# Kernel tuning notes

Measured on AMD Instinct MI355X. Metric: run time of the kernel, lower is better.

## Reference

```python
import jax, jax.numpy as jnp
import numpy as np

H = 16  # heads
D = 1024  # hidden
HD = D // H
FF = 4096
EPS = 1e-12


def _linear_params(key, d_in, d_out):
    k1, k2 = jax.random.split(key)
    bound = 1.0 / np.sqrt(d_in)
    W = jax.random.uniform(k1, (d_in, d_out), minval=-bound, maxval=bound, dtype=jnp.float32)
    b = jax.random.uniform(k2, (d_out,), minval=-bound, maxval=bound, dtype=jnp.float32)
    return W, b


def setup_inputs() -> dict:
    key = jax.random.key(0)
    ks = jax.random.split(key, 8)
    x = jax.random.normal(ks[0], (4, 2048, D), dtype=jnp.float32)
    mask = jnp.ones((4, 1, 1, 2048), dtype=jnp.int32)
    Wq, bq = _linear_params(ks[1], D, D)
    Wk, bk = _linear_params(ks[2], D, D)
    Wv, bv = _linear_params(ks[3], D, D)
    Wo, bo = _linear_params(ks[4], D, D)
    W1, b1 = _linear_params(ks[5], D, FF)
    W2, b2 = _linear_params(ks[6], FF, D)
    g1 = jnp.ones((D,), jnp.float32); be1 = jnp.zeros((D,), jnp.float32)
    g2 = jnp.ones((D,), jnp.float32); be2 = jnp.zeros((D,), jnp.float32)
    return {"x": x, "mask": mask,
            "Wq": Wq, "bq": bq, "Wk": Wk, "bk": bk, "Wv": Wv, "bv": bv,
            "Wo": Wo, "bo": bo, "W1": W1, "b1": b1, "W2": W2, "b2": b2,
            "g1": g1, "be1": be1, "g2": g2, "be2": be2}


def _layernorm(x, g, b):
    mu = jnp.mean(x, axis=-1, keepdims=True)
    var = jnp.mean(jnp.square(x - mu), axis=-1, keepdims=True)
    return (x - mu) / jnp.sqrt(var + EPS) * g + b


def reference(x, mask, Wq, bq, Wk, bk, Wv, bv, Wo, bo, W1, b1, W2, b2, g1, be1, g2, be2):
    B, L, _ = x.shape
    h = _layernorm(x, g1, be1)
    # [B, H, L, HD]
    q = (h @ Wq + bq).reshape(B, L, H, HD).transpose(0, 2, 1, 3)
    k = (h @ Wk + bk).reshape(B, L, H, HD).transpose(0, 2, 1, 3)
    v = (h @ Wv + bv).reshape(B, L, H, HD).transpose(0, 2, 1, 3)
    scores = jnp.einsum('bhqd,bhkd->bhqk', q, k) / np.sqrt(HD).astype(np.float32)
    scores = jnp.where(mask == 0, jnp.float32(-1e9), scores)
    attn = jax.nn.softmax(scores, axis=-1)  # dropout = identity (eval mode)
    out = jnp.einsum('bhqk,bhkd->bhqd', attn, v)
    out = out.transpose(0, 2, 1, 3).reshape(B, L, D)
    x = x + (out @ Wo + bo)
    h = _layernorm(x, g2, be2)
    ff = jax.nn.gelu(h @ W1 + b1, approximate=False) @ W2 + b2
    return x + ff
```

## Files before the change

kernel.cpp:

```cpp
#include <hip/hip_runtime.h>
#include <stdint.h>

#define D_MODEL 1024
#define NHEAD   16
#define HDIM    64
#define FFDIM   4096
#define BATCH   4
#define SEQ     2048
#define ROWS    (BATCH*SEQ)

typedef unsigned short u16;
typedef __bf16 bf16_t;
typedef bf16_t bf16x8 __attribute__((ext_vector_type(8)));
typedef float  f32x4  __attribute__((ext_vector_type(4)));

#define SCQ 0.18033688011112042f

__device__ __forceinline__ u16 f2bf(float f) {
  union { float f; unsigned u; } v; v.f = f;
  unsigned r = v.u + 0x7fffu + ((v.u >> 16) & 1u);
  return (u16)(r >> 16);
}

__device__ __forceinline__ void gl2lds16(const void* g, void* l) {
  __builtin_amdgcn_global_load_lds((const __attribute__((address_space(1))) void*)g,
                                   (__attribute__((address_space(3))) void*)l, 16, 0, 0);
}

#define MFMA_BF16(a, b, c) __builtin_amdgcn_mfma_f32_16x16x32_bf16((a), (b), (c), 0, 0, 0)
#define EXP2(x) __builtin_amdgcn_exp2f(x)

__global__ __launch_bounds__(256) void ln_kernel(const float* __restrict__ x,
                                                 const float* __restrict__ g,
                                                 const float* __restrict__ be,
                                                 u16* __restrict__ out) {
  __shared__ float red[10];
  int row = blockIdx.x;
  int t = threadIdx.x;
  const float* xr = x + (size_t)row * D_MODEL;
  float4 xv = ((const float4*)xr)[t];
  float s  = xv.x + xv.y + xv.z + xv.w;
  float s2 = xv.x*xv.x + xv.y*xv.y + xv.z*xv.z + xv.w*xv.w;
  for (int d = 32; d > 0; d >>= 1) { s += __shfl_down(s, d); s2 += __shfl_down(s2, d); }
  int wid = t >> 6;
  if ((t & 63) == 0) { red[wid*2] = s; red[wid*2+1] = s2; }
  __syncthreads();
  if (t == 0) {
    float a = 0.f, b2 = 0.f;
    for (int i = 0; i < 4; ++i) { a += red[i*2]; b2 += red[i*2+1]; }
    red[8] = a; red[9] = b2;
  }
  __syncthreads();
  float mu  = red[8] * (1.0f / D_MODEL);
  float var = red[9] * (1.0f / D_MODEL) - mu*mu;
  float rstd = rsqrtf(var + 1e-12f);
  float4 gv = ((const float4*)g)[t];
  float4 bv = ((const float4*)be)[t];
  unsigned long long o =
      (unsigned long long)f2bf((xv.x - mu) * rstd * gv.x + bv.x)
    | ((unsigned long long)f2bf((xv.y - mu) * rstd * gv.y + bv.y) << 16)
    | ((unsigned long long)f2bf((xv.z - mu) * rstd * gv.z + bv.z) << 32)
    | ((unsigned long long)f2bf((xv.w - mu) * rstd * gv.w + bv.w) << 48);
  ((unsigned long long*)out)[(size_t)row * (D_MODEL/4) + t] = o;
}

__global__ __launch_bounds__(256) void wt_kernel(const float* __restrict__ W,
                                                 u16* __restrict__ Wt, int K, int N) {
  __shared__ float tile[32][33];
  int n0 = blockIdx.x * 32, k0 = blockIdx.y * 32;
  int tx = threadIdx.x & 31, ty = threadIdx.x >> 5;
  #pragma unroll
  for (int i = 0; i < 4; ++i) {
    int k = ty + i*8;
    tile[k][tx] = W[(size_t)(k0 + k) * N + n0 + tx];
  }
  __syncthreads();
  #pragma unroll
  for (int i = 0; i < 4; ++i) {
    int n = ty + i*8;
    Wt[(size_t)(n0 + n) * K + k0 + tx] = f2bf(tile[tx][n]);
  }
}

__global__ __launch_bounds__(256) void vtrans_kernel(const u16* __restrict__ vb,
                                                     u16* __restrict__ vt) {
  __shared__ __align__(16) u16 tile[64][80];
  int kb = blockIdx.x * 64;
  int bh = blockIdx.y;
  int b = bh >> 4, h = bh & 15;
  int t = threadIdx.x;
  int key = t >> 2, dq = (t & 3) * 16;
  const u16* src = vb + (size_t)b*SEQ*D_MODEL + (size_t)(kb+key)*D_MODEL + h*HDIM + dq;
  *(bf16x8*)&tile[key][dq]     = *(const bf16x8*)(src);
  *(bf16x8*)&tile[key][dq + 8] = *(const bf16x8*)(src + 8);
  __syncthreads();
  int w = t >> 6, lane = t & 63;
  int kq = w * 16;
  u16 vals[16];
  #pragma unroll
  for (int e = 0; e < 16; ++e) vals[e] = tile[kq + e][lane];
  u16* dst = vt + (size_t)bh * HDIM * SEQ + (size_t)lane * SEQ + kb + kq;
  *(bf16x8*)dst       = *(const bf16x8*)&vals[0];
  *(bf16x8*)(dst + 8) = *(const bf16x8*)&vals[8];
}

__device__ __forceinline__ float gelu_f(float v) {
  return 0.5f * v * (1.0f + erff(v * 0.70710678118654752f));
}

template<int EPI>
__global__ __launch_bounds__(512, 2) void gemm256(const u16* __restrict__ A,
                                                  const u16* __restrict__ Bt,
                                                  const float* __restrict__ bias,
                                                  const float* __restrict__ resid,
                                                  void* __restrict__ outp,
                                                  int M, int N, int K,
                                                  const float* __restrict__ bias2,
                                                  const float* __restrict__ bias3,
                                                  void* __restrict__ out2,
                                                  void* __restrict__ out3) {
  __shared__ __align__(16) u16 sA[3][128*64];
  __shared__ __align__(16) u16 sB[3][256*64];
  const int tid = threadIdx.x;
  const int lane = tid & 63, w = tid >> 6;
  const int r = lane & 15, kg = lane >> 4, r7 = r & 7;
  const int wr = w >> 2, wc = w & 3;

  const int gx = gridDim.x;
  const int nwg = gx * gridDim.y;
  const int orig = blockIdx.y * gx + blockIdx.x;
  const int lid = (orig & 7) * (nwg >> 3) + (orig >> 3);
  const int bm = lid / gx, bn = lid % gx;

  const int NT = K >> 6;

  size_t offA[2], offB[4];
  #pragma unroll
  for (int u = 0; u < 2; ++u) {
    int slot = u*512 + tid;
    int row = slot >> 3, g = slot & 7;
    offA[u] = (size_t)(bm*128 + row) * K + ((g ^ (row & 7)) * 8);
  }
  #pragma unroll
  for (int u = 0; u < 4; ++u) {
    int slot = u*512 + tid;
    int row = slot >> 3, g = slot & 7;
    offB[u] = (size_t)(bn*256 + row) * K + ((g ^ (row & 7)) * 8);
  }

  f32x4 acc[4][4];
  #pragma unroll
  for (int m = 0; m < 4; ++m)
    #pragma unroll
    for (int n = 0; n < 4; ++n) acc[m][n] = f32x4{0.f, 0.f, 0.f, 0.f};

  const float* bsel = bias;
  u16* osel = (u16*)outp;
  int bnl = bn;
  float qscale = 1.0f;
  if (EPI == 3) {
    int sec = bn >> 2;
    bsel = (sec == 0) ? bias : (sec == 1 ? bias2 : bias3);
    osel = (u16*)((sec == 0) ? outp : (sec == 1 ? out2 : out3));
    if (sec == 0) qscale = SCQ;
    bnl = bn & 3;
  }
  float bv4[4];
  #pragma unroll
  for (int n = 0; n < 4; ++n) bv4[n] = bsel[bnl*256 + wc*64 + n*16 + r];

  auto load_frags = [&](bf16x8 (&aa)[4], bf16x8 (&bb)[4], int bbuf, int sl) {
    #pragma unroll
    for (int m = 0; m < 4; ++m)
      aa[m] = *(const bf16x8*)&sA[bbuf][(wr*64 + m*16 + r)*64 + (((sl*4 + kg) ^ r7) * 8)];
    #pragma unroll
    for (int n = 0; n < 4; ++n)
      bb[n] = *(const bf16x8*)&sB[bbuf][(wc*64 + n*16 + r)*64 + (((sl*4 + kg) ^ r7) * 8)];
  };
  auto mfma16 = [&](bf16x8 (&aa)[4], bf16x8 (&bb)[4]) {
    __builtin_amdgcn_s_setprio(1);
    #pragma unroll
    for (int m = 0; m < 4; ++m)
      #pragma unroll
      for (int n = 0; n < 4; ++n)
        acc[m][n] = MFMA_BF16(aa[m], bb[n], acc[m][n]);
    __builtin_amdgcn_s_setprio(0);
  };

  #pragma unroll
  for (int u = 0; u < 2; ++u) gl2lds16(A  + offA[u],      &sA[0][(u*512+tid)*8]);
  #pragma unroll
  for (int u = 0; u < 4; ++u) gl2lds16(Bt + offB[u],      &sB[0][(u*512+tid)*8]);
  #pragma unroll
  for (int u = 0; u < 2; ++u) gl2lds16(A  + offA[u] + 64, &sA[1][(u*512+tid)*8]);
  #pragma unroll
  for (int u = 0; u < 4; ++u) gl2lds16(Bt + offB[u] + 64, &sB[1][(u*512+tid)*8]);
  asm volatile("s_waitcnt vmcnt(6)" ::: "memory");
  __builtin_amdgcn_s_barrier();

  bf16x8 a0[4], b0[4], a1[4], b1[4];
  load_frags(a0, b0, 0, 0);

  int buf = 0;
  for (int t = 0; t < NT - 1; ++t) {
    int nb = buf + 2; if (nb >= 3) nb -= 3;
    const bool pre = (t + 2 < NT);
    const size_t koff = (size_t)(t + 2) * 64;

    load_frags(a1, b1, buf, 1);
    if (pre) {
      gl2lds16(A  + offA[0] + koff, &sA[nb][(0*512+tid)*8]);
      gl2lds16(A  + offA[1] + koff, &sA[nb][(1*512+tid)*8]);
      gl2lds16(Bt + offB[0] + koff, &sB[nb][(0*512+tid)*8]);
      gl2lds16(Bt + offB[1] + koff, &sB[nb][(1*512+tid)*8]);
      gl2lds16(Bt + offB[2] + koff, &sB[nb][(2*512+tid)*8]);
      gl2lds16(Bt + offB[3] + koff, &sB[nb][(3*512+tid)*8]);
    }
    mfma16(a0, b0);
    asm volatile("s_waitcnt lgkmcnt(0)" ::: "memory");
    __builtin_amdgcn_sched_barrier(0);
    if (pre) asm volatile("s_waitcnt vmcnt(6)" ::: "memory");
    else     asm volatile("s_waitcnt vmcnt(0)" ::: "memory");
    __builtin_amdgcn_s_barrier();

    int bnext = buf + 1; if (bnext >= 3) bnext -= 3;
    load_frags(a0, b0, bnext, 0);
    mfma16(a1, b1);
    buf = bnext;
  }
  load_frags(a1, b1, buf, 1);
  mfma16(a0, b0);
  mfma16(a1, b1);

  const int orow = bm*128 + wr*64;
  const int ocol = (EPI == 3 ? bnl : bn)*256 + wc*64;
  const int ostride = (EPI == 3) ? 1024 : N;
  #pragma unroll
  for (int m = 0; m < 4; ++m) {
    #pragma unroll
    for (int n = 0; n < 4; ++n) {
      #pragma unroll
      for (int j = 0; j < 4; ++j) {
        int rr = orow + m*16 + kg*4 + j;
        int cc = ocol + n*16 + r;
        size_t idx = (size_t)rr * ostride + cc;
        float v = acc[m][n][j] + bv4[n];
        if (EPI == 0)       ((u16*)outp)[idx]   = f2bf(v);
        else if (EPI == 1)  ((float*)outp)[idx] = resid[idx] + v;
        else if (EPI == 2)  ((u16*)outp)[idx]   = f2bf(gelu_f(v));
        else                osel[idx]           = f2bf(v * qscale);
      }
    }
  }
}

__global__ __launch_bounds__(256) void attn_kernel(const u16* __restrict__ qb,
                                                   const u16* __restrict__ kb,
                                                   const u16* __restrict__ vt,
                                                   const int* __restrict__ mask,
                                                   u16* __restrict__ ob) {
  __shared__ __align__(16) u16 sK[2][64*64];
  __shared__ __align__(16) u16 sV[2][64*64];
  __shared__ __align__(16) bf16_t sP[4][16*64];
  __shared__ unsigned char sOkPart[256];
  __shared__ unsigned sTileOk;
  const float THR2 = 11.541560327111708f;
  int tid = threadIdx.x;
  int lane = tid & 63, w = tid >> 6;
  int r = lane & 15, kg = lane >> 4;
  int r7 = r & 7;
  int qt = blockIdx.x;
  int bh = blockIdx.y;
  int b = bh >> 4, h = bh & 15;
  size_t qkbase = (size_t)b * SEQ * D_MODEL + (size_t)h * HDIM;
  const u16* vtb = vt + (size_t)bh * HDIM * SEQ;
  const int* mrow = mask + b * SEQ;

  {
    int ok = 1;
    #pragma unroll
    for (int e = 0; e < 8; ++e) ok &= (mrow[tid*8 + e] != 0);
    sOkPart[tid] = (unsigned char)ok;
  }
  __syncthreads();
  if (w == 0) {
    int a = 0;
    if (lane < 32) {
      a = 1;
      #pragma unroll
      for (int e = 0; e < 8; ++e) a &= sOkPart[lane*8 + e];
    }
    unsigned long long bits = __ballot(a != 0);
    if (lane == 0) sTileOk = (unsigned)(bits & 0xffffffffu);
  }
  __syncthreads();
  const unsigned tileOkBits = sTileOk;

  const u16* qrow = qb + qkbase + (size_t)(qt*64 + w*16 + r) * D_MODEL + kg*8;
  bf16x8 qf[2];
  qf[0] = *(const bf16x8*)(qrow);
  qf[1] = *(const bf16x8*)(qrow + 32);

  bf16x8 ones;
  {
    bf16_t one = (bf16_t)1.0f;
    #pragma unroll
    for (int e = 0; e < 8; ++e) ones[e] = one;
  }

  f32x4 oacc[4];
  #pragma unroll
  for (int n = 0; n < 4; ++n) oacc[n] = f32x4{0.f, 0.f, 0.f, 0.f};
  f32x4 oaccS = f32x4{0.f, 0.f, 0.f, 0.f};
  float m_run[4] = {-1e30f, -1e30f, -1e30f, -1e30f};

  int ch0 = w*64 + lane, ch1 = ch0 + 256;
  int row0 = ch0 >> 3, col0 = ((ch0 & 7) ^ (row0 & 7)) * 8;
  int row1 = ch1 >> 3, col1 = ((ch1 & 7) ^ (row1 & 7)) * 8;
  const u16* kp0 = kb + qkbase + (size_t)row0 * D_MODEL + col0;
  const u16* kp1 = kb + qkbase + (size_t)row1 * D_MODEL + col1;
  const u16* vp0 = vtb + (size_t)row0 * SEQ + col0;
  const u16* vp1 = vtb + (size_t)row1 * SEQ + col1;

  const int NT = SEQ / 64;

  gl2lds16(kp0, &sK[0][ch0*8]);
  gl2lds16(kp1, &sK[0][ch1*8]);
  gl2lds16(vp0, &sV[0][ch0*8]);
  gl2lds16(vp1, &sV[0][ch1*8]);
  kp0 += 64*D_MODEL; kp1 += 64*D_MODEL; vp0 += 64; vp1 += 64;

  #pragma unroll 2
  for (int kt = 0; kt < NT; ++kt) {
    int cur = kt & 1;
    int key0 = kt * 64;
    if (kt + 1 < NT) {
      gl2lds16(kp0, &sK[cur^1][ch0*8]);
      gl2lds16(kp1, &sK[cur^1][ch1*8]);
      gl2lds16(vp0, &sV[cur^1][ch0*8]);
      gl2lds16(vp1, &sV[cur^1][ch1*8]);
      kp0 += 64*D_MODEL; kp1 += 64*D_MODEL; vp0 += 64; vp1 += 64;
      asm volatile("s_waitcnt vmcnt(4)" ::: "memory");
    } else {
      asm volatile("s_waitcnt vmcnt(0)" ::: "memory");
    }
    __builtin_amdgcn_s_barrier();

    const u16* Kt = sK[cur];
    const u16* Vt = sV[cur];

    f32x4 s[4];
    #pragma unroll
    for (int n = 0; n < 4; ++n) s[n] = f32x4{0.f, 0.f, 0.f, 0.f};
    #pragma unroll
    for (int c = 0; c < 2; ++c) {
      #pragma unroll
      for (int n = 0; n < 4; ++n) {
        bf16x8 kf = *(const bf16x8*)&Kt[(n*16 + r)*64 + (((c*4 + kg) ^ r7) * 8)];
        s[n] = MFMA_BF16(qf[c], kf, s[n]);
      }
    }

    if (!((tileOkBits >> kt) & 1u)) {
      int mk[4];
      #pragma unroll
      for (int n = 0; n < 4; ++n) mk[n] = mrow[key0 + n*16 + r];
      #pragma unroll
      for (int n = 0; n < 4; ++n)
        #pragma unroll
        for (int j = 0; j < 4; ++j)
          s[n][j] = mk[n] ? s[n][j] : -1e9f;
    }
    float tm[4];
    #pragma unroll
    for (int n = 0; n < 4; ++n)
      #pragma unroll
      for (int j = 0; j < 4; ++j)
        tm[j] = (n == 0) ? s[n][j] : fmaxf(tm[j], s[n][j]);

    bool grow = (tm[0] > m_run[0] + THR2) | (tm[1] > m_run[1] + THR2) |
                (tm[2] > m_run[2] + THR2) | (tm[3] > m_run[3] + THR2);
    if (__any(grow)) {
      #pragma unroll
      for (int d = 1; d < 16; d <<= 1) {
        #pragma unroll
        for (int j = 0; j < 4; ++j) tm[j] = fmaxf(tm[j], __shfl_xor(tm[j], d));
      }
      #pragma unroll
      for (int j = 0; j < 4; ++j) {
        float mn = fmaxf(m_run[j], tm[j]);
        float al = EXP2(m_run[j] - mn);
        m_run[j] = mn;
        oaccS[j] *= al;
        oacc[0][j] *= al; oacc[1][j] *= al; oacc[2][j] *= al; oacc[3][j] *= al;
      }
    }
    bf16_t* pw = sP[w];
    #pragma unroll
    for (int n = 0; n < 4; ++n) {
      int cg = n*2 + (r >> 3);
      #pragma unroll
      for (int j = 0; j < 4; ++j) {
        float p = EXP2(s[n][j] - m_run[j]);
        int row = kg*4 + j;
        pw[row*64 + ((cg ^ (row & 7)) * 8) + r7] = (bf16_t)p;
      }
    }
    bf16x8 pa[2];
    #pragma unroll
    for (int c = 0; c < 2; ++c)
      pa[c] = *(const bf16x8*)&sP[w][r*64 + (((c*4 + kg) ^ r7) * 8)];
    #pragma unroll
    for (int c = 0; c < 2; ++c) {
      #pragma unroll
      for (int n = 0; n < 4; ++n) {
        bf16x8 vf = *(const bf16x8*)&Vt[(n*16 + r)*64 + (((c*4 + kg) ^ r7) * 8)];
        oacc[n] = MFMA_BF16(pa[c], vf, oacc[n]);
      }
      oaccS = MFMA_BF16(pa[c], ones, oaccS);
    }
    __builtin_amdgcn_s_barrier();
  }

  float rcp[4];
  #pragma unroll
  for (int j = 0; j < 4; ++j) rcp[j] = 1.0f / oaccS[j];
  #pragma unroll
  for (int n = 0; n < 4; ++n) {
    #pragma unroll
    for (int j = 0; j < 4; ++j) {
      int q = qt*64 + w*16 + kg*4 + j;
      int d = h*HDIM + n*16 + r;
      ob[(size_t)(b*SEQ + q) * D_MODEL + d] = f2bf(oacc[n][j] * rcp[j]);
    }
  }
}

extern "C" void kernel_launch(void* const* d_in, const int* in_sizes, int n_in,
                              void* d_out, int out_size, void* d_ws, size_t ws_size,
                              hipStream_t stream) {
  const float* x   = (const float*)d_in[0];
  const int*  mask = (const int*)d_in[1];
  const float* Wq = (const float*)d_in[2];  const float* bq = (const float*)d_in[3];
  const float* Wk = (const float*)d_in[4];  const float* bk = (const float*)d_in[5];
  const float* Wv = (const float*)d_in[6];  const float* bv = (const float*)d_in[7];
  const float* Wo = (const float*)d_in[8];  const float* bo = (const float*)d_in[9];
  const float* W1 = (const float*)d_in[10]; const float* b1 = (const float*)d_in[11];
  const float* W2 = (const float*)d_in[12]; const float* b2 = (const float*)d_in[13];
  const float* g1 = (const float*)d_in[14]; const float* be1 = (const float*)d_in[15];
  const float* g2 = (const float*)d_in[16]; const float* be2 = (const float*)d_in[17];

  const size_t MB = 1u << 20;
  char* ws = (char*)d_ws;
  u16*  hln  = (u16*)(ws);
  u16*  vt   = (u16*)(ws);
  u16*  qb   = (u16*)(ws + 16*MB);
  u16*  kb   = (u16*)(ws + 32*MB);
  u16*  vb   = (u16*)(ws + 48*MB);
  u16*  attn = (u16*)(ws + 64*MB);
  u16*  ff1  = (u16*)(ws + 16*MB);
  float* x2  = (float*)(ws + 80*MB);
  u16*  WqkvT= (u16*)(ws + 112*MB);
  u16*  WqT  = WqkvT;
  u16*  WkT  = (u16*)(ws + 114*MB);
  u16*  WvT  = (u16*)(ws + 116*MB);
  u16*  WoT  = (u16*)(ws + 118*MB);
  u16*  W1T  = (u16*)(ws + 120*MB);
  u16*  W2T  = (u16*)(ws + 128*MB);

  dim3 tb(256);
  wt_kernel<<<dim3(1024/32, 1024/32), tb, 0, stream>>>(Wq, WqT, 1024, 1024);
  wt_kernel<<<dim3(1024/32, 1024/32), tb, 0, stream>>>(Wk, WkT, 1024, 1024);
  wt_kernel<<<dim3(1024/32, 1024/32), tb, 0, stream>>>(Wv, WvT, 1024, 1024);
  wt_kernel<<<dim3(1024/32, 1024/32), tb, 0, stream>>>(Wo, WoT, 1024, 1024);
  wt_kernel<<<dim3(4096/32, 1024/32), tb, 0, stream>>>(W1, W1T, 1024, 4096);
  wt_kernel<<<dim3(1024/32, 4096/32), tb, 0, stream>>>(W2, W2T, 4096, 1024);

  ln_kernel<<<ROWS, tb, 0, stream>>>(x, g1, be1, hln);

  dim3 gb(512);
  gemm256<3><<<dim3(3072/256, ROWS/128), gb, 0, stream>>>(hln, WqkvT, bq, nullptr, qb,
                                                          ROWS, 3072, 1024,
                                                          bk, bv, kb, vb);

  vtrans_kernel<<<dim3(SEQ/64, BATCH*NHEAD), tb, 0, stream>>>(vb, vt);

  attn_kernel<<<dim3(SEQ/64, BATCH*NHEAD), tb, 0, stream>>>(qb, kb, vt, mask, attn);

  gemm256<1><<<dim3(1024/256, ROWS/128), gb, 0, stream>>>(attn, WoT, bo, x, x2,
                                                          ROWS, 1024, 1024,
                                                          nullptr, nullptr, nullptr, nullptr);

  ln_kernel<<<ROWS, tb, 0, stream>>>(x2, g2, be2, hln);

  gemm256<2><<<dim3(4096/256, ROWS/128), gb, 0, stream>>>(hln, W1T, b1, nullptr, ff1,
                                                          ROWS, 4096, 1024,
                                                          nullptr, nullptr, nullptr, nullptr);

  gemm256<1><<<dim3(1024/256, ROWS/128), gb, 0, stream>>>(ff1, W2T, b2, x2, (float*)d_out,
                                                          ROWS, 1024, 4096,
                                                          nullptr, nullptr, nullptr, nullptr);
}
```

Baseline: 428.5 us.

## Restructure attention to 32x32 MFMA with register-resident P and 128-query tiles

Rewrites the attention kernel to compute S^T with 32x32x16 bf16 MFMAs, so each wave owns 32 query rows and a block covers 128 queries. The probabilities are packed to bf16 in registers and exchanged with permlane32 swaps instead of round-tripping through LDS. The row sum is kept as a scalar instead of an extra MFMA against ones. The aim is to halve K/V tile reloads per query and to remove the LDS traffic and per-tile sync for P. In exchange, the grid has half as many blocks, registers are heavier, and the rescale factors go through a small LDS buffer.

```diff
diff --git a/kernel.cpp b/kernel.cpp
--- a/kernel.cpp
+++ b/kernel.cpp
@@ -13,6 +13,7 @@
 typedef __bf16 bf16_t;
 typedef bf16_t bf16x8 __attribute__((ext_vector_type(8)));
 typedef float  f32x4  __attribute__((ext_vector_type(4)));
+typedef float  f32x16 __attribute__((ext_vector_type(16)));
 
 #define SCQ 0.18033688011112042f
 
@@ -28,7 +29,14 @@
 }
 
 #define MFMA_BF16(a, b, c) __builtin_amdgcn_mfma_f32_16x16x32_bf16((a), (b), (c), 0, 0, 0)
+#define MFMA32(a, b, c)    __builtin_amdgcn_mfma_f32_32x32x16_bf16((a), (b), (c), 0, 0, 0)
 #define EXP2(x) __builtin_amdgcn_exp2f(x)
+
+__device__ __forceinline__ bf16x8 mk8(unsigned a, unsigned b, unsigned c, unsigned d) {
+  union { unsigned u[4]; bf16x8 v; } t;
+  t.u[0] = a; t.u[1] = b; t.u[2] = c; t.u[3] = d;
+  return t.v;
+}
 
 __global__ __launch_bounds__(256) void ln_kernel(const float* __restrict__ x,
                                                  const float* __restrict__ g,
@@ -254,21 +262,20 @@
   }
 }
 
-__global__ __launch_bounds__(256) void attn_kernel(const u16* __restrict__ qb,
-                                                   const u16* __restrict__ kb,
-                                                   const u16* __restrict__ vt,
-                                                   const int* __restrict__ mask,
-                                                   u16* __restrict__ ob) {
+__global__ __launch_bounds__(256, 4) void attn_kernel(const u16* __restrict__ qb,
+                                                      const u16* __restrict__ kb,
+                                                      const u16* __restrict__ vt,
+                                                      const int* __restrict__ mask,
+                                                      u16* __restrict__ ob) {
   __shared__ __align__(16) u16 sK[2][64*64];
   __shared__ __align__(16) u16 sV[2][64*64];
-  __shared__ __align__(16) bf16_t sP[4][16*64];
+  __shared__ float sAl[4][32];
   __shared__ unsigned char sOkPart[256];
   __shared__ unsigned sTileOk;
   const float THR2 = 11.541560327111708f;
   int tid = threadIdx.x;
   int lane = tid & 63, w = tid >> 6;
-  int r = lane & 15, kg = lane >> 4;
-  int r7 = r & 7;
+  int l31 = lane & 31, hi = lane >> 5;
   int qt = blockIdx.x;
   int bh = blockIdx.y;
   int b = bh >> 4, h = bh & 15;
@@ -296,23 +303,17 @@
   __syncthreads();
   const unsigned tileOkBits = sTileOk;
 
-  const u16* qrow = qb + qkbase + (size_t)(qt*64 + w*16 + r) * D_MODEL + kg*8;
-  bf16x8 qf[2];
-  qf[0] = *(const bf16x8*)(qrow);
-  qf[1] = *(const bf16x8*)(qrow + 32);
-
-  bf16x8 ones;
-  {
-    bf16_t one = (bf16_t)1.0f;
-    #pragma unroll
-    for (int e = 0; e < 8; ++e) ones[e] = one;
-  }
-
-  f32x4 oacc[4];
-  #pragma unroll
-  for (int n = 0; n < 4; ++n) oacc[n] = f32x4{0.f, 0.f, 0.f, 0.f};
-  f32x4 oaccS = f32x4{0.f, 0.f, 0.f, 0.f};
-  float m_run[4] = {-1e30f, -1e30f, -1e30f, -1e30f};
+  const u16* qrow = qb + qkbase + (size_t)(qt*128 + w*32 + l31) * D_MODEL + hi*8;
+  bf16x8 qf[4];
+  #pragma unroll
+  for (int dstep = 0; dstep < 4; ++dstep)
+    qf[dstep] = *(const bf16x8*)(qrow + dstep*16);
+
+  f32x16 oacc0, oacc1;
+  #pragma unroll
+  for (int e = 0; e < 16; ++e) { oacc0[e] = 0.f; oacc1[e] = 0.f; }
+  float m_run = -1e30f;
+  float lsum  = 0.f;
 
   int ch0 = w*64 + lane, ch1 = ch0 + 256;
   int row0 = ch0 >> 3, col0 = ((ch0 & 7) ^ (row0 & 7)) * 8;
@@ -330,7 +331,6 @@
   gl2lds16(vp1, &sV[0][ch1*8]);
   kp0 += 64*D_MODEL; kp1 += 64*D_MODEL; vp0 += 64; vp1 += 64;
 
-  #pragma unroll 2
   for (int kt = 0; kt < NT; ++kt) {
     int cur = kt & 1;
     int key0 = kt * 64;
@@ -349,90 +349,102 @@
     const u16* Kt = sK[cur];
     const u16* Vt = sV[cur];
 
-    f32x4 s[4];
-    #pragma unroll
-    for (int n = 0; n < 4; ++n) s[n] = f32x4{0.f, 0.f, 0.f, 0.f};
-    #pragma unroll
-    for (int c = 0; c < 2; ++c) {
+    f32x16 s0, s1;
+    #pragma unroll
+    for (int e = 0; e < 16; ++e) { s0[e] = 0.f; s1[e] = 0.f; }
+    #pragma unroll
+    for (int dstep = 0; dstep < 4; ++dstep) {
+      int g = dstep*2 + hi;
+      bf16x8 kf0 = *(const bf16x8*)&Kt[l31*64        + ((g ^ (l31 & 7)) * 8)];
+      bf16x8 kf1 = *(const bf16x8*)&Kt[(32 + l31)*64 + ((g ^ ((32 + l31) & 7)) * 8)];
+      s0 = MFMA32(kf0, qf[dstep], s0);
+      s1 = MFMA32(kf1, qf[dstep], s1);
+    }
+
+    if (!((tileOkBits >> kt) & 1u)) {
       #pragma unroll
-      for (int n = 0; n < 4; ++n) {
-        bf16x8 kf = *(const bf16x8*)&Kt[(n*16 + r)*64 + (((c*4 + kg) ^ r7) * 8)];
-        s[n] = MFMA_BF16(qf[c], kf, s[n]);
+      for (int reg = 0; reg < 16; ++reg) {
+        int kr = (reg & 3) + 8*(reg >> 2) + 4*hi;
+        if (!mrow[key0 + kr])      s0[reg] = -1e9f;
+        if (!mrow[key0 + 32 + kr]) s1[reg] = -1e9f;
       }
     }
 
-    if (!((tileOkBits >> kt) & 1u)) {
-      int mk[4];
+    float tm = s0[0];
+    #pragma unroll
+    for (int e = 1; e < 16; ++e) tm = fmaxf(tm, s0[e]);
+    #pragma unroll
+    for (int e = 0; e < 16; ++e) tm = fmaxf(tm, s1[e]);
+    tm = fmaxf(tm, __shfl_xor(tm, 32));
+
+    if (__any(tm > m_run + THR2)) {
+      float mn = fmaxf(m_run, tm);
+      float al = EXP2(m_run - mn);
+      m_run = mn;
+      lsum *= al;
+      if (lane < 32) sAl[w][lane] = al;
+      asm volatile("s_waitcnt lgkmcnt(0)" ::: "memory");
       #pragma unroll
-      for (int n = 0; n < 4; ++n) mk[n] = mrow[key0 + n*16 + r];
-      #pragma unroll
-      for (int n = 0; n < 4; ++n)
-        #pragma unroll
-        for (int j = 0; j < 4; ++j)
-          s[n][j] = mk[n] ? s[n][j] : -1e9f;
-    }
-    float tm[4];
-    #pragma unroll
-    for (int n = 0; n < 4; ++n)
-      #pragma unroll
-      for (int j = 0; j < 4; ++j)
-        tm[j] = (n == 0) ? s[n][j] : fmaxf(tm[j], s[n][j]);
-
-    bool grow = (tm[0] > m_run[0] + THR2) | (tm[1] > m_run[1] + THR2) |
-                (tm[2] > m_run[2] + THR2) | (tm[3] > m_run[3] + THR2);
-    if (__any(grow)) {
-      #pragma unroll
-      for (int d = 1; d < 16; d <<= 1) {
-        #pragma unroll
-        for (int j = 0; j < 4; ++j) tm[j] = fmaxf(tm[j], __shfl_xor(tm[j], d));
+      for (int reg = 0; reg < 16; ++reg) {
+        float a2 = sAl[w][(reg & 3) + 8*(reg >> 2) + 4*hi];
+        oacc0[reg] *= a2; oacc1[reg] *= a2;
       }
-      #pragma unroll
-      for (int j = 0; j < 4; ++j) {
-        float mn = fmaxf(m_run[j], tm[j]);
-        float al = EXP2(m_run[j] - mn);
-        m_run[j] = mn;
-        oaccS[j] *= al;
-        oacc[0][j] *= al; oacc[1][j] *= al; oacc[2][j] *= al; oacc[3][j] *= al;
-      }
-    }
-    bf16_t* pw = sP[w];
-    #pragma unroll
-    for (int n = 0; n < 4; ++n) {
-      int cg = n*2 + (r >> 3);
-      #pragma unroll
-      for (int j = 0; j < 4; ++j) {
-        float p = EXP2(s[n][j] - m_run[j]);
-        int row = kg*4 + j;
-        pw[row*64 + ((cg ^ (row & 7)) * 8) + r7] = (bf16_t)p;
-      }
-    }
-    bf16x8 pa[2];
-    #pragma unroll
-    for (int c = 0; c < 2; ++c)
-      pa[c] = *(const bf16x8*)&sP[w][r*64 + (((c*4 + kg) ^ r7) * 8)];
-    #pragma unroll
-    for (int c = 0; c < 2; ++c) {
-      #pragma unroll
-      for (int n = 0; n < 4; ++n) {
-        bf16x8 vf = *(const bf16x8*)&Vt[(n*16 + r)*64 + (((c*4 + kg) ^ r7) * 8)];
-        oacc[n] = MFMA_BF16(pa[c], vf, oacc[n]);
-      }
-      oaccS = MFMA_BF16(pa[c], ones, oaccS);
+    }
+
+    #pragma unroll
+    for (int e = 0; e < 16; ++e) {
+      s0[e] = EXP2(s0[e] - m_run); lsum += s0[e];
+      s1[e] = EXP2(s1[e] - m_run); lsum += s1[e];
+    }
+
+    unsigned wa, wb, wc, wd, we, wf, wg, wh;
+#define CVTPK(dst, lo_, hi_) asm("v_cvt_pk_bf16_f32 %0, %1, %2" : "=v"(dst) : "v"(lo_), "v"(hi_))
+    CVTPK(wa, s0[0],  s0[1]);  CVTPK(wb, s0[2],  s0[3]);
+    CVTPK(wc, s0[4],  s0[5]);  CVTPK(wd, s0[6],  s0[7]);
+    CVTPK(we, s0[8],  s0[9]);  CVTPK(wf, s0[10], s0[11]);
+    CVTPK(wg, s0[12], s0[13]); CVTPK(wh, s0[14], s0[15]);
+    asm volatile("v_permlane32_swap_b32 %0, %1" : "+v"(wc), "+v"(wa));
+    asm volatile("v_permlane32_swap_b32 %0, %1" : "+v"(wd), "+v"(wb));
+    asm volatile("v_permlane32_swap_b32 %0, %1" : "+v"(wg), "+v"(we));
+    asm volatile("v_permlane32_swap_b32 %0, %1" : "+v"(wh), "+v"(wf));
+    bf16x8 pa0 = mk8(wa, wb, wc, wd);
+    bf16x8 pa1 = mk8(we, wf, wg, wh);
+    CVTPK(wa, s1[0],  s1[1]);  CVTPK(wb, s1[2],  s1[3]);
+    CVTPK(wc, s1[4],  s1[5]);  CVTPK(wd, s1[6],  s1[7]);
+    CVTPK(we, s1[8],  s1[9]);  CVTPK(wf, s1[10], s1[11]);
+    CVTPK(wg, s1[12], s1[13]); CVTPK(wh, s1[14], s1[15]);
+    asm volatile("v_permlane32_swap_b32 %0, %1" : "+v"(wc), "+v"(wa));
+    asm volatile("v_permlane32_swap_b32 %0, %1" : "+v"(wd), "+v"(wb));
+    asm volatile("v_permlane32_swap_b32 %0, %1" : "+v"(wg), "+v"(we));
+    asm volatile("v_permlane32_swap_b32 %0, %1" : "+v"(wh), "+v"(wf));
+    bf16x8 pa2 = mk8(wa, wb, wc, wd);
+    bf16x8 pa3 = mk8(we, wf, wg, wh);
+#undef CVTPK
+
+    int r0 = l31, r1 = 32 + l31;
+    #pragma unroll
+    for (int kstep = 0; kstep < 4; ++kstep) {
+      int g = kstep*2 + hi;
+      bf16x8 vf0 = *(const bf16x8*)&Vt[r0*64 + ((g ^ (r0 & 7)) * 8)];
+      bf16x8 vf1 = *(const bf16x8*)&Vt[r1*64 + ((g ^ (r1 & 7)) * 8)];
+      bf16x8 pk = (kstep == 0) ? pa0 : (kstep == 1) ? pa1 : (kstep == 2) ? pa2 : pa3;
+      oacc0 = MFMA32(pk, vf0, oacc0);
+      oacc1 = MFMA32(pk, vf1, oacc1);
     }
     __builtin_amdgcn_s_barrier();
   }
 
-  float rcp[4];
-  #pragma unroll
-  for (int j = 0; j < 4; ++j) rcp[j] = 1.0f / oaccS[j];
-  #pragma unroll
-  for (int n = 0; n < 4; ++n) {
-    #pragma unroll
-    for (int j = 0; j < 4; ++j) {
-      int q = qt*64 + w*16 + kg*4 + j;
-      int d = h*HDIM + n*16 + r;
-      ob[(size_t)(b*SEQ + q) * D_MODEL + d] = f2bf(oacc[n][j] * rcp[j]);
-    }
+  float lsumT = lsum + __shfl_xor(lsum, 32);
+  if (lane < 32) sAl[w][lane] = 1.0f / lsumT;
+  asm volatile("s_waitcnt lgkmcnt(0)" ::: "memory");
+  #pragma unroll
+  for (int reg = 0; reg < 16; ++reg) {
+    int qr = (reg & 3) + 8*(reg >> 2) + 4*hi;
+    float rc = sAl[w][qr];
+    int qg = qt*128 + w*32 + qr;
+    size_t base2 = (size_t)(b*SEQ + qg) * D_MODEL + h*HDIM + l31;
+    ob[base2]      = f2bf(oacc0[reg] * rc);
+    ob[base2 + 32] = f2bf(oacc1[reg] * rc);
   }
 }
 
@@ -485,7 +497,7 @@
 
   vtrans_kernel<<<dim3(SEQ/64, BATCH*NHEAD), tb, 0, stream>>>(vb, vt);
 
-  attn_kernel<<<dim3(SEQ/64, BATCH*NHEAD), tb, 0, stream>>>(qb, kb, vt, mask, attn);
+  attn_kernel<<<dim3(SEQ/128, BATCH*NHEAD), tb, 0, stream>>>(qb, kb, vt, mask, attn);
 
   gemm256<1><<<dim3(1024/256, ROWS/128), gb, 0, stream>>>(attn, WoT, bo, x, x2,
                                                           ROWS, 1024, 1024,
```

After: 387.8 us. -9.5%, faster.
